# Optimization experiments

Hardware: AMD Instinct MI355X
Metric: run time of the kernel (lower is better)

The kernel has to match this reference:

```python
import jax, jax.numpy as jnp
import numpy as np

N_ATOMS = 200000
AEV_DIM = 384
H1, H2, H3 = 160, 128, 96
N_SPECIES = 4
ALPHA = 0.1  # CELU alpha used by ANI atomic networks


def setup_inputs() -> dict:
    key = jax.random.key(0)
    ks = jax.random.split(key, 8)
    aev = jax.random.normal(ks[0], (N_ATOMS, AEV_DIM), dtype=jnp.float32)
    # Disjoint species partition (matches (species==s).nonzero() buffers)
    perm = jax.random.permutation(ks[1], N_ATOMS)
    chunk = N_ATOMS // N_SPECIES
    H_idx = perm[0 * chunk:1 * chunk]
    C_idx = perm[1 * chunk:2 * chunk]
    N_idx = perm[2 * chunk:3 * chunk]
    O_idx = perm[3 * chunk:4 * chunk]

    def init(k, shape, fan_in):
        return (jax.random.normal(k, shape, dtype=jnp.float32) / np.float32(np.sqrt(fan_in)))

    # Stacked per-species MLP params: leading axis = species (H,C,N,O)
    W1 = init(ks[2], (N_SPECIES, AEV_DIM, H1), AEV_DIM); b1 = jnp.zeros((N_SPECIES, H1), jnp.float32)
    W2 = init(ks[3], (N_SPECIES, H1, H2), H1);          b2 = jnp.zeros((N_SPECIES, H2), jnp.float32)
    W3 = init(ks[4], (N_SPECIES, H2, H3), H2);          b3 = jnp.zeros((N_SPECIES, H3), jnp.float32)
    W4 = init(ks[5], (N_SPECIES, H3, 1), H3);           b4 = jnp.zeros((N_SPECIES, 1), jnp.float32)
    return {"aev": aev,
            "W1": W1, "b1": b1, "W2": W2, "b2": b2,
            "W3": W3, "b3": b3, "W4": W4, "b4": b4,
            "H_idx": H_idx, "C_idx": C_idx, "N_idx": N_idx, "O_idx": O_idx}


def _species_mlp(x, W1, b1, W2, b2, W3, b3, W4, b4):
    h = jax.nn.celu(x @ W1 + b1, ALPHA)
    h = jax.nn.celu(h @ W2 + b2, ALPHA)
    h = jax.nn.celu(h @ W3 + b3, ALPHA)
    return (h @ W4 + b4).reshape(-1)  # per-atom scalar energy


def reference(aev, W1, b1, W2, b2, W3, b3, W4, b4, H_idx, C_idx, N_idx, O_idx):
    out = jnp.zeros((aev.shape[0],), dtype=aev.dtype)
    # Fixed small loop over the 4 species networks (structurally distinct experts)
    for s, idx in enumerate((H_idx, C_idx, N_idx, O_idx)):
        e = _species_mlp(aev[idx], W1[s], b1[s], W2[s], b2[s], W3[s], b3[s], W4[s], b4[s])
        out = out.at[idx].add(e)  # index_add_ scatter
    # output.unsqueeze(0).sum(dim=1) -> molecular energy, shape [1]
    return out[None, :].sum(axis=1)
```

## Files before the change

### kernel.cpp

```cpp
#include <hip/hip_runtime.h>

#define DI __device__ __forceinline__

constexpr int AEV = 384;
constexpr int H1N = 160;
constexpr int H2N = 128;
constexpr int H3N = 96;
constexpr int NSP = 4;
constexpr int W1P = 392;
constexpr int W2P = 168;
constexpr int W3P = 136;
constexpr int NMAX = 200000;

using half8  = __attribute__((ext_vector_type(8))) _Float16;
using half4v = __attribute__((ext_vector_type(4))) _Float16;
using f32x4  = __attribute__((ext_vector_type(4))) float;

__device__ __align__(16) _Float16 g_w1[NSP * H1N * AEV];
__device__ __align__(16) _Float16 g_w2[NSP * H2N * H1N];
__device__ __align__(16) _Float16 g_w3[NSP * H3N * H2N];
__device__ __align__(16) _Float16 g_h1[(size_t)NMAX * H1N];

DI float celu_f(float x) {
  return fmaxf(x, 0.f) + 0.1f * (exp2f(fminf(x, 0.f) * 14.426950408889634f) - 1.f);
}
DI f32x4 mfma16h(half8 a, half8 b, f32x4 c) {
  return __builtin_amdgcn_mfma_f32_16x16x32_f16(a, b, c, 0, 0, 0);
}
DI half8 cvt8(float4 a, float4 b) {
  half8 t;
  t[0] = (_Float16)a.x; t[1] = (_Float16)a.y; t[2] = (_Float16)a.z; t[3] = (_Float16)a.w;
  t[4] = (_Float16)b.x; t[5] = (_Float16)b.y; t[6] = (_Float16)b.z; t[7] = (_Float16)b.w;
  return t;
}

template <int K, int N>
DI void tp(const float* __restrict__ src, _Float16* dst, int id) {
  constexpr int per = K * N;
  int s = id / per, r = id % per;
  int n = r / K, k = r % K;
  dst[s * per + n * K + k] = (_Float16)src[s * per + k * N + n];
}

__global__ void prep(const float* __restrict__ W1, const float* __restrict__ W2,
                     const float* __restrict__ W3, float* __restrict__ out) {
  int id = blockIdx.x * 256 + threadIdx.x;
  if (id == 0) out[0] = 0.f;
  constexpr int E1 = NSP * AEV * H1N;
  constexpr int E2 = NSP * H1N * H2N;
  constexpr int E3 = NSP * H2N * H3N;
  if (id < E1)                 tp<AEV, H1N>(W1, g_w1, id);
  else if (id < E1 + E2)       tp<H1N, H2N>(W2, g_w2, id - E1);
  else if (id < E1 + E2 + E3)  tp<H2N, H3N>(W3, g_w3, id - E1 - E2);
}

__global__ __launch_bounds__(1024, 4) void layer1_k(
    const float* __restrict__ aev, const float* __restrict__ b1,
    const int* __restrict__ i0, const int* __restrict__ i1,
    const int* __restrict__ i2, const int* __restrict__ i3,
    int chunk) {
  __shared__ __align__(16) _Float16 W1s[H1N * W1P];

  const int tid  = threadIdx.x;
  const int lane = tid & 63, wav = tid >> 6;
  const int l15  = lane & 15, quad = lane >> 4;
  const int s    = blockIdx.y;
  const int* idx = (s == 0) ? i0 : (s == 1) ? i1 : (s == 2) ? i2 : i3;

  const _Float16* wsrc = g_w1 + (size_t)s * H1N * AEV;
#pragma unroll
  for (int i = 0; i < 8; ++i) {
    int c = tid + i * 1024;
    if (c < H1N * (AEV / 8)) {
      int n = c / (AEV / 8), kc = c % (AEV / 8);
      *(half8*)(W1s + n * W1P + kc * 8) = *(const half8*)(wsrc + n * AEV + kc * 8);
    }
  }
  __syncthreads();

  const int a = blockIdx.x * 256 + wav * 16 + l15;
  const bool valid = (a < chunk);
  const int r = idx[valid ? a : (chunk - 1)];
  const float* xr = aev + (size_t)r * AEV + quad * 8;

  f32x4 acc[10];
#pragma unroll
  for (int m = 0; m < 10; ++m)
#pragma unroll
    for (int i = 0; i < 4; ++i) acc[m][i] = 0.f;

  float4 xf0 = *(const float4*)(xr), xf1 = *(const float4*)(xr + 4);
#pragma unroll
  for (int ks = 0; ks < 12; ++ks) {
    half8 bv = cvt8(xf0, xf1);
    if (ks < 11) {
      xf0 = *(const float4*)(xr + (ks + 1) * 32);
      xf1 = *(const float4*)(xr + (ks + 1) * 32 + 4);
    }
#pragma unroll
    for (int mt = 0; mt < 10; ++mt) {
      half8 aw = *(const half8*)(W1s + (mt * 16 + l15) * W1P + ks * 32 + quad * 8);
      acc[mt] = mfma16h(aw, bv, acc[mt]);
    }
  }
  _Float16* hrow = g_h1 + ((size_t)s * chunk + a) * H1N;
#pragma unroll
  for (int mt = 0; mt < 10; ++mt) {
    float4 bb = *(const float4*)(b1 + s * H1N + mt * 16 + quad * 4);
    half4v o;
    o[0] = (_Float16)celu_f(acc[mt][0] + bb.x);
    o[1] = (_Float16)celu_f(acc[mt][1] + bb.y);
    o[2] = (_Float16)celu_f(acc[mt][2] + bb.z);
    o[3] = (_Float16)celu_f(acc[mt][3] + bb.w);
    if (valid) *(half4v*)(hrow + mt * 16 + quad * 4) = o;
  }
}

__global__ __launch_bounds__(1024, 4) void layer234_k(
    const float* __restrict__ b2, const float* __restrict__ b3,
    const float* __restrict__ W4, const float* __restrict__ pb4,
    int chunk, float* __restrict__ out) {
  __shared__ __align__(16) _Float16 W2s[H2N * W2P];
  __shared__ __align__(16) _Float16 W3s[H3N * W3P];
  __shared__ __align__(16) _Float16 H2s[16 * 16 * W3P];
  __shared__ float RED[16];

  const int tid  = threadIdx.x;
  const int lane = tid & 63, wav = tid >> 6;
  const int l15  = lane & 15, quad = lane >> 4;
  const int s    = blockIdx.y;

  const _Float16* w2src = g_w2 + (size_t)s * H2N * H1N;
  const _Float16* w3src = g_w3 + (size_t)s * H3N * H2N;
#pragma unroll
  for (int i = 0; i < 3; ++i) {
    int c = tid + i * 1024;
    if (c < H2N * (H1N / 8)) {
      int n = c / (H1N / 8), kc = c % (H1N / 8);
      *(half8*)(W2s + n * W2P + kc * 8) = *(const half8*)(w2src + n * H1N + kc * 8);
    }
  }
#pragma unroll
  for (int i = 0; i < 2; ++i) {
    int c = tid + i * 1024;
    if (c < H3N * (H2N / 8)) {
      int n = c / (H2N / 8), kc = c % (H2N / 8);
      *(half8*)(W3s + n * W3P + kc * 8) = *(const half8*)(w3src + n * H2N + kc * 8);
    }
  }
  __syncthreads();

  const int a = blockIdx.x * 256 + wav * 16 + l15;
  const bool valid = (a < chunk);
  const int ac = valid ? a : (chunk - 1);
  const _Float16* hrow = g_h1 + ((size_t)s * chunk + ac) * H1N + quad * 8;
  _Float16* H2w = H2s + wav * (16 * W3P);

  half8 bv2[5];
#pragma unroll
  for (int ks = 0; ks < 5; ++ks) bv2[ks] = *(const half8*)(hrow + ks * 32);
  f32x4 acc2[8];
#pragma unroll
  for (int m = 0; m < 8; ++m)
#pragma unroll
    for (int i = 0; i < 4; ++i) acc2[m][i] = 0.f;
#pragma unroll
  for (int mt = 0; mt < 8; ++mt)
#pragma unroll
    for (int ks = 0; ks < 5; ++ks) {
      half8 aw = *(const half8*)(W2s + (mt * 16 + l15) * W2P + ks * 32 + quad * 8);
      acc2[mt] = mfma16h(aw, bv2[ks], acc2[mt]);
    }
#pragma unroll
  for (int mt = 0; mt < 8; ++mt) {
    float4 bb = *(const float4*)(b2 + s * H2N + mt * 16 + quad * 4);
    half4v o;
    o[0] = (_Float16)celu_f(acc2[mt][0] + bb.x);
    o[1] = (_Float16)celu_f(acc2[mt][1] + bb.y);
    o[2] = (_Float16)celu_f(acc2[mt][2] + bb.z);
    o[3] = (_Float16)celu_f(acc2[mt][3] + bb.w);
    *(half4v*)(H2w + l15 * W3P + mt * 16 + quad * 4) = o;
  }

  half8 bv3[4];
#pragma unroll
  for (int ks = 0; ks < 4; ++ks)
    bv3[ks] = *(const half8*)(H2w + l15 * W3P + ks * 32 + quad * 8);
  f32x4 acc3[6];
#pragma unroll
  for (int m = 0; m < 6; ++m)
#pragma unroll
    for (int i = 0; i < 4; ++i) acc3[m][i] = 0.f;
#pragma unroll
  for (int mt = 0; mt < 6; ++mt)
#pragma unroll
    for (int ks = 0; ks < 4; ++ks) {
      half8 aw = *(const half8*)(W3s + (mt * 16 + l15) * W3P + ks * 32 + quad * 8);
      acc3[mt] = mfma16h(aw, bv3[ks], acc3[mt]);
    }
#pragma unroll
  for (int mt = 0; mt < 6; ++mt) {
    float4 bb = *(const float4*)(b3 + s * H3N + mt * 16 + quad * 4);
    half4v o;
    o[0] = (_Float16)celu_f(acc3[mt][0] + bb.x);
    o[1] = (_Float16)celu_f(acc3[mt][1] + bb.y);
    o[2] = (_Float16)celu_f(acc3[mt][2] + bb.z);
    o[3] = (_Float16)celu_f(acc3[mt][3] + bb.w);
    *(half4v*)(H2w + l15 * W3P + mt * 16 + quad * 4) = o;
  }

  float e = 0.f;
  {
    const _Float16* h3 = H2w + l15 * W3P + quad * 24;
    const float* w4 = W4 + s * H3N + quad * 24;
#pragma unroll
    for (int j = 0; j < 3; ++j) {
      half8 hv = *(const half8*)(h3 + j * 8);
      float4 wa = *(const float4*)(w4 + j * 8);
      float4 wb = *(const float4*)(w4 + j * 8 + 4);
      e += (float)hv[0] * wa.x + (float)hv[1] * wa.y + (float)hv[2] * wa.z + (float)hv[3] * wa.w
         + (float)hv[4] * wb.x + (float)hv[5] * wb.y + (float)hv[6] * wb.z + (float)hv[7] * wb.w;
    }
  }
  e += __shfl_xor(e, 16, 64);
  e += __shfl_xor(e, 32, 64);
  e = (lane < 16 && valid) ? (e + pb4[s]) : 0.f;
#pragma unroll
  for (int off = 8; off > 0; off >>= 1) e += __shfl_xor(e, off, 64);
  if (lane == 0) RED[wav] = e;
  __syncthreads();
  if (tid == 0) {
    float t = 0.f;
#pragma unroll
    for (int i = 0; i < 16; ++i) t += RED[i];
    atomicAdd(out, t);
  }
}

extern "C" void kernel_launch(void* const* d_in, const int* in_sizes, int n_in,
                              void* d_out, int out_size, void* d_ws, size_t ws_size,
                              hipStream_t stream) {
  (void)n_in; (void)d_ws; (void)ws_size; (void)out_size;
  const float* aev = (const float*)d_in[0];
  const float* W1  = (const float*)d_in[1];
  const float* b1  = (const float*)d_in[2];
  const float* W2  = (const float*)d_in[3];
  const float* b2  = (const float*)d_in[4];
  const float* W3  = (const float*)d_in[5];
  const float* b3  = (const float*)d_in[6];
  const float* W4  = (const float*)d_in[7];
  const float* b4  = (const float*)d_in[8];
  const int* iH = (const int*)d_in[9];
  const int* iC = (const int*)d_in[10];
  const int* iN = (const int*)d_in[11];
  const int* iO = (const int*)d_in[12];
  const int chunk = in_sizes[9];

  constexpr int TOT = NSP * (AEV * H1N + H1N * H2N + H2N * H3N);
  prep<<<TOT / 256, 256, 0, stream>>>(W1, W2, W3, (float*)d_out);

  const int tiles = (chunk + 255) / 256;
  layer1_k<<<dim3(tiles, NSP), 1024, 0, stream>>>(aev, b1, iH, iC, iN, iO, chunk);
  layer234_k<<<dim3(tiles, NSP), 1024, 0, stream>>>(b2, b3, W4, b4, chunk, (float*)d_out);
}
```

Before: 512.1 us.

## Fuse all MLP layers into one kernel, keeping activations in registers

```diff
diff --git a/kernel.cpp b/kernel.cpp
--- a/kernel.cpp
+++ b/kernel.cpp
@@ -7,10 +7,10 @@
 constexpr int H2N = 128;
 constexpr int H3N = 96;
 constexpr int NSP = 4;
-constexpr int W1P = 392;
+constexpr int W1P = 200;
 constexpr int W2P = 168;
 constexpr int W3P = 136;
-constexpr int NMAX = 200000;
+constexpr int W3OFF = H2N * W2P;
 
 using half8  = __attribute__((ext_vector_type(8))) _Float16;
 using half4v = __attribute__((ext_vector_type(4))) _Float16;
@@ -19,7 +19,6 @@
 __device__ __align__(16) _Float16 g_w1[NSP * H1N * AEV];
 __device__ __align__(16) _Float16 g_w2[NSP * H2N * H1N];
 __device__ __align__(16) _Float16 g_w3[NSP * H3N * H2N];
-__device__ __align__(16) _Float16 g_h1[(size_t)NMAX * H1N];
 
 DI float celu_f(float x) {
   return fmaxf(x, 0.f) + 0.1f * (exp2f(fminf(x, 0.f) * 14.426950408889634f) - 1.f);
@@ -32,6 +31,24 @@
   t[0] = (_Float16)a.x; t[1] = (_Float16)a.y; t[2] = (_Float16)a.z; t[3] = (_Float16)a.w;
   t[4] = (_Float16)b.x; t[5] = (_Float16)b.y; t[6] = (_Float16)b.z; t[7] = (_Float16)b.w;
   return t;
+}
+DI half4v shfl4(half4v v, int src) {
+  union { half4v h; int i[2]; } u;
+  u.h = v;
+  u.i[0] = __shfl(u.i[0], src, 64);
+  u.i[1] = __shfl(u.i[1], src, 64);
+  return u.h;
+}
+DI half8 bfrag(const half4v* hb, int ks, int l15, int quad) {
+  const int sLo = (quad & 1) * 32 + l15, sHi = sLo + 16;
+  half4v loA = shfl4(hb[2 * ks], sLo),     loB = shfl4(hb[2 * ks + 1], sLo);
+  half4v hiA = shfl4(hb[2 * ks], sHi),     hiB = shfl4(hb[2 * ks + 1], sHi);
+  half4v lo = (quad & 2) ? loB : loA;
+  half4v hi = (quad & 2) ? hiB : hiA;
+  half8 b;
+  b[0] = lo[0]; b[1] = lo[1]; b[2] = lo[2]; b[3] = lo[3];
+  b[4] = hi[0]; b[5] = hi[1]; b[6] = hi[2]; b[7] = hi[3];
+  return b;
 }
 
 template <int K, int N>
@@ -54,12 +71,16 @@
   else if (id < E1 + E2 + E3)  tp<H2N, H3N>(W3, g_w3, id - E1 - E2);
 }
 
-__global__ __launch_bounds__(1024, 4) void layer1_k(
-    const float* __restrict__ aev, const float* __restrict__ b1,
+__global__ __launch_bounds__(512, 4) void fused_mlp(
+    const float* __restrict__ aev,
+    const float* __restrict__ b1, const float* __restrict__ b2,
+    const float* __restrict__ b3,
+    const float* __restrict__ W4, const float* __restrict__ pb4,
     const int* __restrict__ i0, const int* __restrict__ i1,
     const int* __restrict__ i2, const int* __restrict__ i3,
-    int chunk) {
-  __shared__ __align__(16) _Float16 W1s[H1N * W1P];
+    int chunk, float* __restrict__ out) {
+  __shared__ __align__(16) _Float16 WS[34560];
+  __shared__ float RED[8];
 
   const int tid  = threadIdx.x;
   const int lane = tid & 63, wav = tid >> 6;
@@ -67,22 +88,23 @@
   const int s    = blockIdx.y;
   const int* idx = (s == 0) ? i0 : (s == 1) ? i1 : (s == 2) ? i2 : i3;
 
-  const _Float16* wsrc = g_w1 + (size_t)s * H1N * AEV;
-#pragma unroll
-  for (int i = 0; i < 8; ++i) {
-    int c = tid + i * 1024;
-    if (c < H1N * (AEV / 8)) {
-      int n = c / (AEV / 8), kc = c % (AEV / 8);
-      *(half8*)(W1s + n * W1P + kc * 8) = *(const half8*)(wsrc + n * AEV + kc * 8);
-    }
-  }
-  __syncthreads();
-
-  const int a = blockIdx.x * 256 + wav * 16 + l15;
+  const int a = blockIdx.x * 128 + wav * 16 + l15;
   const bool valid = (a < chunk);
   const int r = idx[valid ? a : (chunk - 1)];
   const float* xr = aev + (size_t)r * AEV + quad * 8;
 
+  const _Float16* w1src = g_w1 + (size_t)s * H1N * AEV;
+
+#pragma unroll
+  for (int i = 0; i < 8; ++i) {
+    int c = tid + i * 512;
+    if (c < H1N * 24) {
+      int n = c / 24, kc = c % 24;
+      *(half8*)(WS + n * W1P + kc * 8) = *(const half8*)(w1src + n * AEV + kc * 8);
+    }
+  }
+  __syncthreads();
+
   f32x4 acc[10];
 #pragma unroll
   for (int m = 0; m < 10; ++m)
@@ -91,7 +113,28 @@
 
   float4 xf0 = *(const float4*)(xr), xf1 = *(const float4*)(xr + 4);
 #pragma unroll
-  for (int ks = 0; ks < 12; ++ks) {
+  for (int ks = 0; ks < 6; ++ks) {
+    half8 bv = cvt8(xf0, xf1);
+    xf0 = *(const float4*)(xr + (ks + 1) * 32);
+    xf1 = *(const float4*)(xr + (ks + 1) * 32 + 4);
+#pragma unroll
+    for (int mt = 0; mt < 10; ++mt) {
+      half8 aw = *(const half8*)(WS + (mt * 16 + l15) * W1P + ks * 32 + quad * 8);
+      acc[mt] = mfma16h(aw, bv, acc[mt]);
+    }
+  }
+  __syncthreads();
+#pragma unroll
+  for (int i = 0; i < 8; ++i) {
+    int c = tid + i * 512;
+    if (c < H1N * 24) {
+      int n = c / 24, kc = c % 24;
+      *(half8*)(WS + n * W1P + kc * 8) = *(const half8*)(w1src + 192 + n * AEV + kc * 8);
+    }
+  }
+  __syncthreads();
+#pragma unroll
+  for (int ks = 6; ks < 12; ++ks) {
     half8 bv = cvt8(xf0, xf1);
     if (ks < 11) {
       xf0 = *(const float4*)(xr + (ks + 1) * 32);
@@ -99,11 +142,11 @@
     }
 #pragma unroll
     for (int mt = 0; mt < 10; ++mt) {
-      half8 aw = *(const half8*)(W1s + (mt * 16 + l15) * W1P + ks * 32 + quad * 8);
+      half8 aw = *(const half8*)(WS + (mt * 16 + l15) * W1P + (ks - 6) * 32 + quad * 8);
       acc[mt] = mfma16h(aw, bv, acc[mt]);
     }
   }
-  _Float16* hrow = g_h1 + ((size_t)s * chunk + a) * H1N;
+  half4v hb[10];
 #pragma unroll
   for (int mt = 0; mt < 10; ++mt) {
     float4 bb = *(const float4*)(b1 + s * H1N + mt * 16 + quad * 4);
@@ -112,65 +155,43 @@
     o[1] = (_Float16)celu_f(acc[mt][1] + bb.y);
     o[2] = (_Float16)celu_f(acc[mt][2] + bb.z);
     o[3] = (_Float16)celu_f(acc[mt][3] + bb.w);
-    if (valid) *(half4v*)(hrow + mt * 16 + quad * 4) = o;
-  }
-}
-
-__global__ __launch_bounds__(1024, 4) void layer234_k(
-    const float* __restrict__ b2, const float* __restrict__ b3,
-    const float* __restrict__ W4, const float* __restrict__ pb4,
-    int chunk, float* __restrict__ out) {
-  __shared__ __align__(16) _Float16 W2s[H2N * W2P];
-  __shared__ __align__(16) _Float16 W3s[H3N * W3P];
-  __shared__ __align__(16) _Float16 H2s[16 * 16 * W3P];
-  __shared__ float RED[16];
-
-  const int tid  = threadIdx.x;
-  const int lane = tid & 63, wav = tid >> 6;
-  const int l15  = lane & 15, quad = lane >> 4;
-  const int s    = blockIdx.y;
-
-  const _Float16* w2src = g_w2 + (size_t)s * H2N * H1N;
-  const _Float16* w3src = g_w3 + (size_t)s * H3N * H2N;
-#pragma unroll
-  for (int i = 0; i < 3; ++i) {
-    int c = tid + i * 1024;
-    if (c < H2N * (H1N / 8)) {
-      int n = c / (H1N / 8), kc = c % (H1N / 8);
-      *(half8*)(W2s + n * W2P + kc * 8) = *(const half8*)(w2src + n * H1N + kc * 8);
-    }
-  }
-#pragma unroll
-  for (int i = 0; i < 2; ++i) {
-    int c = tid + i * 1024;
-    if (c < H3N * (H2N / 8)) {
-      int n = c / (H2N / 8), kc = c % (H2N / 8);
-      *(half8*)(W3s + n * W3P + kc * 8) = *(const half8*)(w3src + n * H2N + kc * 8);
-    }
-  }
-  __syncthreads();
-
-  const int a = blockIdx.x * 256 + wav * 16 + l15;
-  const bool valid = (a < chunk);
-  const int ac = valid ? a : (chunk - 1);
-  const _Float16* hrow = g_h1 + ((size_t)s * chunk + ac) * H1N + quad * 8;
-  _Float16* H2w = H2s + wav * (16 * W3P);
-
-  half8 bv2[5];
-#pragma unroll
-  for (int ks = 0; ks < 5; ++ks) bv2[ks] = *(const half8*)(hrow + ks * 32);
+    hb[mt] = o;
+  }
+
+  __syncthreads();
+  {
+    const _Float16* w2src = g_w2 + (size_t)s * H2N * H1N;
+    const _Float16* w3src = g_w3 + (size_t)s * H3N * H2N;
+#pragma unroll
+    for (int i = 0; i < 5; ++i) {
+      int c = tid + i * 512;
+      int n = c / 20, kc = c % 20;
+      *(half8*)(WS + n * W2P + kc * 8) = *(const half8*)(w2src + n * H1N + kc * 8);
+    }
+#pragma unroll
+    for (int i = 0; i < 3; ++i) {
+      int c = tid + i * 512;
+      int n = c / 16, kc = c % 16;
+      *(half8*)(WS + W3OFF + n * W3P + kc * 8) = *(const half8*)(w3src + n * H2N + kc * 8);
+    }
+  }
+  __syncthreads();
+
   f32x4 acc2[8];
 #pragma unroll
   for (int m = 0; m < 8; ++m)
 #pragma unroll
     for (int i = 0; i < 4; ++i) acc2[m][i] = 0.f;
 #pragma unroll
-  for (int mt = 0; mt < 8; ++mt)
-#pragma unroll
-    for (int ks = 0; ks < 5; ++ks) {
-      half8 aw = *(const half8*)(W2s + (mt * 16 + l15) * W2P + ks * 32 + quad * 8);
-      acc2[mt] = mfma16h(aw, bv2[ks], acc2[mt]);
-    }
+  for (int ks = 0; ks < 5; ++ks) {
+    half8 bv = bfrag(hb, ks, l15, quad);
+#pragma unroll
+    for (int mt = 0; mt < 8; ++mt) {
+      half8 aw = *(const half8*)(WS + (mt * 16 + l15) * W2P + ks * 32 + quad * 8);
+      acc2[mt] = mfma16h(aw, bv, acc2[mt]);
+    }
+  }
+  half4v hb2[8];
 #pragma unroll
   for (int mt = 0; mt < 8; ++mt) {
     float4 bb = *(const float4*)(b2 + s * H2N + mt * 16 + quad * 4);
@@ -179,60 +200,45 @@
     o[1] = (_Float16)celu_f(acc2[mt][1] + bb.y);
     o[2] = (_Float16)celu_f(acc2[mt][2] + bb.z);
     o[3] = (_Float16)celu_f(acc2[mt][3] + bb.w);
-    *(half4v*)(H2w + l15 * W3P + mt * 16 + quad * 4) = o;
-  }
-
-  half8 bv3[4];
-#pragma unroll
-  for (int ks = 0; ks < 4; ++ks)
-    bv3[ks] = *(const half8*)(H2w + l15 * W3P + ks * 32 + quad * 8);
+    hb2[mt] = o;
+  }
+
   f32x4 acc3[6];
 #pragma unroll
   for (int m = 0; m < 6; ++m)
 #pragma unroll
     for (int i = 0; i < 4; ++i) acc3[m][i] = 0.f;
 #pragma unroll
-  for (int mt = 0; mt < 6; ++mt)
-#pragma unroll
-    for (int ks = 0; ks < 4; ++ks) {
-      half8 aw = *(const half8*)(W3s + (mt * 16 + l15) * W3P + ks * 32 + quad * 8);
-      acc3[mt] = mfma16h(aw, bv3[ks], acc3[mt]);
-    }
+  for (int ks = 0; ks < 4; ++ks) {
+    half8 bv = bfrag(hb2, ks, l15, quad);
+#pragma unroll
+    for (int mt = 0; mt < 6; ++mt) {
+      half8 aw = *(const half8*)(WS + W3OFF + (mt * 16 + l15) * W3P + ks * 32 + quad * 8);
+      acc3[mt] = mfma16h(aw, bv, acc3[mt]);
+    }
+  }
+
+  float e = 0.f;
 #pragma unroll
   for (int mt = 0; mt < 6; ++mt) {
     float4 bb = *(const float4*)(b3 + s * H3N + mt * 16 + quad * 4);
-    half4v o;
-    o[0] = (_Float16)celu_f(acc3[mt][0] + bb.x);
-    o[1] = (_Float16)celu_f(acc3[mt][1] + bb.y);
-    o[2] = (_Float16)celu_f(acc3[mt][2] + bb.z);
-    o[3] = (_Float16)celu_f(acc3[mt][3] + bb.w);
-    *(half4v*)(H2w + l15 * W3P + mt * 16 + quad * 4) = o;
-  }
-
-  float e = 0.f;
-  {
-    const _Float16* h3 = H2w + l15 * W3P + quad * 24;
-    const float* w4 = W4 + s * H3N + quad * 24;
-#pragma unroll
-    for (int j = 0; j < 3; ++j) {
-      half8 hv = *(const half8*)(h3 + j * 8);
-      float4 wa = *(const float4*)(w4 + j * 8);
-      float4 wb = *(const float4*)(w4 + j * 8 + 4);
-      e += (float)hv[0] * wa.x + (float)hv[1] * wa.y + (float)hv[2] * wa.z + (float)hv[3] * wa.w
-         + (float)hv[4] * wb.x + (float)hv[5] * wb.y + (float)hv[6] * wb.z + (float)hv[7] * wb.w;
-    }
+    float4 wv = *(const float4*)(W4 + s * H3N + mt * 16 + quad * 4);
+    e += (float)(_Float16)celu_f(acc3[mt][0] + bb.x) * wv.x
+       + (float)(_Float16)celu_f(acc3[mt][1] + bb.y) * wv.y
+       + (float)(_Float16)celu_f(acc3[mt][2] + bb.z) * wv.z
+       + (float)(_Float16)celu_f(acc3[mt][3] + bb.w) * wv.w;
   }
   e += __shfl_xor(e, 16, 64);
   e += __shfl_xor(e, 32, 64);
   e = (lane < 16 && valid) ? (e + pb4[s]) : 0.f;
 #pragma unroll
-  for (int off = 8; off > 0; off >>= 1) e += __shfl_xor(e, off, 64);
+  for (int off = 1; off < 64; off <<= 1) e += __shfl_xor(e, off, 64);
   if (lane == 0) RED[wav] = e;
   __syncthreads();
   if (tid == 0) {
     float t = 0.f;
 #pragma unroll
-    for (int i = 0; i < 16; ++i) t += RED[i];
+    for (int i = 0; i < 8; ++i) t += RED[i];
     atomicAdd(out, t);
   }
 }
@@ -259,7 +265,7 @@
   constexpr int TOT = NSP * (AEV * H1N + H1N * H2N + H2N * H3N);
   prep<<<TOT / 256, 256, 0, stream>>>(W1, W2, W3, (float*)d_out);
 
-  const int tiles = (chunk + 255) / 256;
-  layer1_k<<<dim3(tiles, NSP), 1024, 0, stream>>>(aev, b1, iH, iC, iN, iO, chunk);
-  layer234_k<<<dim3(tiles, NSP), 1024, 0, stream>>>(b2, b3, W4, b4, chunk, (float*)d_out);
-}
+  const int tiles = (chunk + 127) / 128;
+  fused_mlp<<<dim3(tiles, NSP), 512, 0, stream>>>(aev, b1, b2, b3, W4, b4,
+                                                  iH, iC, iN, iO, chunk, (float*)d_out);
+}
```

Measured after the change: 478.1 us. 1.07x faster.
